# Optimization experiments

Hardware: AMD Instinct MI355X
Metric: run time of the kernel (lower is better)

The kernel has to match this reference:

```python
import jax, jax.numpy as jnp
import numpy as np

LAMDA = 0.05
BETA = 1.0
FULL = 256          # full image / k-space size
SAMP = 128          # sampled k-space size
OFF_R, OFF_C = 3, 3 # sampling offsets from cop.Sample(3, 3, ...)
IR = (OFF_R + 2 * jnp.arange(SAMP)) % FULL  # row sample indices (stride 2)
IC = (OFF_C + 2 * jnp.arange(SAMP)) % FULL  # col sample indices


def dwt2(x):
    # single-level orthonormal 2D Haar DWT, quadrant layout [LL LH; HL HH]
    a = x[..., ::2, ::2]; b = x[..., ::2, 1::2]
    c = x[..., 1::2, ::2]; d = x[..., 1::2, 1::2]
    ll = (a + b + c + d) * 0.5
    lh = (a - b + c - d) * 0.5
    hl = (a + b - c - d) * 0.5
    hh = (a - b - c + d) * 0.5
    top = jnp.concatenate([ll, lh], axis=-1)
    bot = jnp.concatenate([hl, hh], axis=-1)
    return jnp.concatenate([top, bot], axis=-2)


def idwt2(w):
    H = w.shape[-2] // 2; W = w.shape[-1] // 2
    ll = w[..., :H, :W]; lh = w[..., :H, W:]
    hl = w[..., H:, :W]; hh = w[..., H:, W:]
    a = (ll + lh + hl + hh) * 0.5
    b = (ll - lh + hl - hh) * 0.5
    c = (ll + lh - hl - hh) * 0.5
    d = (ll - lh - hl + hh) * 0.5
    x = jnp.zeros(w.shape, w.dtype)
    x = x.at[..., ::2, ::2].set(a)
    x = x.at[..., ::2, 1::2].set(b)
    x = x.at[..., 1::2, ::2].set(c)
    x = x.at[..., 1::2, 1::2].set(d)
    return x


def shrink(x, t):
    # soft-thresholding (prox of t*|x|_1)
    return jnp.sign(x) * jnp.maximum(jnp.abs(x) - t, 0.0)


def sample(x):
    # gather strided k-space samples: [..., 256, 256] -> [..., 128, 128]
    return x[..., IR[:, None], IC[None, :]]


def sample_t(v):
    # adjoint: scatter samples back into zero-filled full grid
    full = jnp.zeros(v.shape[:-2] + (FULL, FULL), v.dtype)
    return full.at[..., IR[:, None], IC[None, :]].set(v)


def setup_inputs() -> dict:
    key = jax.random.key(0)
    k1, k2 = jax.random.split(key)
    s = jax.random.normal(k1, (256, SAMP, SAMP), dtype=jnp.float32)
    image = jax.random.normal(k2, (256, FULL, FULL), dtype=jnp.float32)
    return {"s": s, "image": image}


def reference(s, image):
    thresh = 1.0 / BETA
    coeff = LAMDA / BETA
    dwt_x = dwt2(image)
    new_alpha = shrink(dwt_x, thresh)
    # new_v = dwt_x - new_alpha; idwt(new_alpha - new_v) = idwt(2*alpha - dwt_x)
    idwtx = idwt2(2.0 * new_alpha - dwt_x)
    y = jnp.fft.fft2(idwtx) + coeff * sample_t(s)
    y = y + coeff * sample_t(sample(y))
    return jnp.fft.ifft2(y)
```

## Files before the change

kernel.cpp:

```cpp
#include <hip/hip_runtime.h>


__device__ __forceinline__ float fwv(float w) {
    float sh = fmaxf(fabsf(w) - 1.0f, 0.0f);
    return 2.0f * copysignf(sh, w) - w;
}

__device__ __forceinline__ int bitrev7(int x) {
    return (int)(__builtin_bitreverse32((unsigned)x) >> 25);
}

__global__ __launch_bounds__(1024, 4) void fused_kernel(const float* __restrict__ s,
                                                        const float* __restrict__ image,
                                                        float* __restrict__ outf)
{
    __shared__ float2 A[128 * 128];
    __shared__ float2 ph_tab[256];

    const int tid  = threadIdx.x;
    const int lane = tid & 63;
    const int wave = tid >> 6;
    const int b    = blockIdx.x;
    const float PI_F   = 3.14159265358979323846f;
    const float TWO_PI = 6.2831853071795864769f;

    const float2* ib2 = (const float2*)(image + (size_t)b * 65536);
    const int q  = tid & 63;
    const int pw = tid >> 6;
    float2 img[4][8];
    #pragma unroll
    for (int it = 0; it < 4; ++it) {
        int p = (it << 4) | pw;
        #pragma unroll
        for (int Aq = 0; Aq < 2; ++Aq)
            #pragma unroll
            for (int Bq = 0; Bq < 2; ++Bq)
                #pragma unroll
                for (int r = 0; r < 2; ++r)
                    img[it][(Aq << 2) | (Bq << 1) | r] =
                        ib2[(2 * (p + 64 * Aq) + r) * 128 + (q + 64 * Bq)];
    }

    if (tid < 256) {
        float ps, pc;
        __sincosf((TWO_PI * 3.0f / 256.0f) * (float)tid, &ps, &pc);
        ph_tab[tid] = make_float2(pc, ps);
    }

    float twc[7], tws[7];
    #pragma unroll
    for (int k = 0; k < 7; ++k) {
        int h = 64 >> k;
        float th = PI_F * (float)(lane & (h - 1)) / (float)h;
        __sincosf(th, &tws[k], &twc[k]);
    }

#define FFT128()                                                                     \
    do {                                                                             \
        { float ar = x0r, ai = x0i, br = x1r, bi = x1i;                              \
          x0r = ar + br; x0i = ai + bi;                                              \
          float dr = ar - br, di = ai - bi;                                          \
          x1r = dr * twc[0] - di * tws[0];                                           \
          x1i = dr * tws[0] + di * twc[0]; }                                         \
        _Pragma("unroll")                                                            \
        for (int k = 1; k < 7; ++k) {                                                \
            int h = 64 >> k;                                                         \
            bool hi = (lane & h) != 0;                                               \
            float wc = twc[k], ws = tws[k];                                          \
            { float rr = __shfl_xor(x0r, h), ri = __shfl_xor(x0i, h);                \
              float sr = hi ? (rr - x0r) : (x0r + rr);                               \
              float si = hi ? (ri - x0i) : (x0i + ri);                               \
              float tr = sr * wc - si * ws, ti = sr * ws + si * wc;                  \
              x0r = hi ? tr : sr; x0i = hi ? ti : si; }                              \
            { float rr = __shfl_xor(x1r, h), ri = __shfl_xor(x1i, h);                \
              float sr = hi ? (rr - x1r) : (x1r + rr);                               \
              float si = hi ? (ri - x1i) : (x1i + ri);                               \
              float tr = sr * wc - si * ws, ti = sr * ws + si * wc;                  \
              x1r = hi ? tr : sr; x1i = hi ? ti : si; }                              \
        }                                                                            \
    } while (0)

    const float* sb = s + (size_t)b * (128 * 128);
    const int p0 = lane, p1 = 64 | lane;

    const int m6   = (int)(__builtin_bitreverse32((unsigned)lane) >> 26);
    const int prt0 = (int)(__builtin_bitreverse32((unsigned)((64 - m6) & 63)) >> 26);

    #pragma unroll 2
    for (int t = 0; t < 4; ++t) {
        int ia = (wave << 3) | (t << 1);
        int ic = ia | 1;
        float x0r = sb[ia * 128 + lane];
        float x0i = sb[ic * 128 + lane];
        float x1r = sb[ia * 128 + 64 + lane];
        float x1i = sb[ic * 128 + 64 + lane];
        FFT128();
        float c0r = __shfl(x0r, prt0), c0i = __shfl(x0i, prt0);
        float a0r = 0.5f * (x0r + c0r), a0i = 0.5f * (x0i - c0i);
        float b0r = 0.5f * (x0i + c0i), b0i = 0.5f * (c0r - x0r);
        float c1r = __shfl_xor(x1r, 63), c1i = __shfl_xor(x1i, 63);
        float a1r = 0.5f * (x1r + c1r), a1i = 0.5f * (x1i - c1i);
        float b1r = 0.5f * (x1i + c1i), b1i = 0.5f * (c1r - x1r);
        A[p0 * 128 + ((ia ^ p0) & 127)] = make_float2(a0r, a0i);
        A[p0 * 128 + ((ic ^ p0) & 127)] = make_float2(b0r, b0i);
        A[p1 * 128 + ((ia ^ p1) & 127)] = make_float2(a1r, a1i);
        A[p1 * 128 + ((ic ^ p1) & 127)] = make_float2(b1r, b1i);
    }
    __syncthreads();

    #pragma unroll 2
    for (int t = 0; t < 8; ++t) {
        int vp = (wave << 3) | t;
        float2 a0 = A[vp * 128 + ((p0 ^ vp) & 127)];
        float2 a1 = A[vp * 128 + ((p1 ^ vp) & 127)];
        float x0r = a0.x, x0i = a0.y, x1r = a1.x, x1i = a1.y;
        FFT128();
        A[vp * 128 + ((p0 ^ vp) & 127)] = make_float2(x0r, x0i);
        A[vp * 128 + ((p1 ^ vp) & 127)] = make_float2(x1r, x1i);
    }
    __syncthreads();

    const float  c0    = 0.0125f;
    const float  kappa = 0.0525f / 65536.0f;
    const size_t obase = (size_t)b * 65536;
    const int rv0 = bitrev7(2 * q), rv1 = bitrev7(2 * q + 1);

    #pragma unroll
    for (int it = 0; it < 4; ++it) {
        int p = (it << 4) | pw;

        float D[2][2][2][2];
        #pragma unroll
        for (int Aq = 0; Aq < 2; ++Aq) {
            #pragma unroll
            for (int Bq = 0; Bq < 2; ++Bq) {
                float2 t0 = img[it][(Aq << 2) | (Bq << 1)];
                float2 t1 = img[it][(Aq << 2) | (Bq << 1) | 1];
                float a = t0.x, bb = t0.y, cc = t1.x, dd = t1.y;
                float wll = (a + bb + cc + dd) * 0.5f;
                float wlh = (a - bb + cc - dd) * 0.5f;
                float whl = (a + bb - cc - dd) * 0.5f;
                float whh = (a - bb - cc + dd) * 0.5f;
                float vll = fwv(wll), vlh = fwv(wlh), vhl = fwv(whl), vhh = fwv(whh);
                D[Aq][Bq][0][0] = (vll + vlh + vhl + vhh) * 0.5f;
                D[Aq][Bq][0][1] = (vll - vlh + vhl - vhh) * 0.5f;
                D[Aq][Bq][1][0] = (vll + vlh - vhl - vhh) * 0.5f;
                D[Aq][Bq][1][1] = (vll - vlh - vhl + vhh) * 0.5f;
            }
        }
        float S[2][2];
        #pragma unroll
        for (int r = 0; r < 2; ++r)
            #pragma unroll
            for (int c = 0; c < 2; ++c)
                S[r][c] = D[0][0][r][c] - D[1][0][r][c] - D[0][1][r][c] + D[1][1][r][c];

        int ru0 = bitrev7(2 * p), ru1 = bitrev7(2 * p + 1);
        float2 Tv[2][2];
        Tv[0][0] = A[rv0 * 128 + ((ru0 ^ rv0) & 127)];
        Tv[0][1] = A[rv1 * 128 + ((ru0 ^ rv1) & 127)];
        Tv[1][0] = A[rv0 * 128 + ((ru1 ^ rv0) & 127)];
        Tv[1][1] = A[rv1 * 128 + ((ru1 ^ rv1) & 127)];

        int tbase = 2 * p + 2 * q;
        float2 phv[3] = { ph_tab[tbase], ph_tab[tbase + 1], ph_tab[tbase + 2] };

        #pragma unroll
        for (int Aq = 0; Aq < 2; ++Aq) {
            #pragma unroll
            for (int Bq = 0; Bq < 2; ++Bq) {
                float kq = ((Aq + Bq) & 1) ? -kappa : kappa;
                float sS = ((Aq ^ Bq) & 1) ? -c0 : c0;
                int nrow = 2 * p + 128 * Aq;
                int mcol = 2 * q + 128 * Bq;
                #pragma unroll
                for (int r = 0; r < 2; ++r) {
                    float2 ph0 = phv[r];
                    float2 ph1 = phv[r + 1];
                    float2 wv;
                    wv.x = D[Aq][Bq][r][0] + sS * S[r][0]
                         + kq * (ph0.x * Tv[r][0].x - ph0.y * Tv[r][0].y);
                    wv.y = D[Aq][Bq][r][1] + sS * S[r][1]
                         + kq * (ph1.x * Tv[r][1].x - ph1.y * Tv[r][1].y);
                    *(float2*)&outf[obase + (size_t)((nrow + r) * 256 + mcol)] = wv;
                }
            }
        }
    }
#undef FFT128
}

extern "C" void kernel_launch(void* const* d_in, const int* in_sizes, int n_in,
                              void* d_out, int out_size, void* d_ws, size_t ws_size,
                              hipStream_t stream)
{
    const float* s     = (const float*)d_in[0];
    const float* image = (const float*)d_in[1];
    float*       outf  = (float*)d_out;
    hipLaunchKernelGGL(fused_kernel, dim3(256), dim3(1024), 0, stream,
                       s, image, outf);
}
```

Baseline: 138.8 us.

## Exploit Hermitian symmetry to halve second-pass FFTs and split image loads

The row FFT pass stores only the non-redundant half of each row's spectrum, the column FFT pass runs on only half the rows (paired real columns packed into a complex FFT), and the output stage reads mirrored entries with conjugate sign flips. The image load is split in two: half is loaded up front and the other half after the FFT stage, and the wavelet/shrink work for the first half is computed before the column FFTs. The aim is to halve column-FFT work and reduce register pressure, at the cost of more complex indexing and a special-case branch for the DC/Nyquist pair.

Result: faster. 133.9 us (-3.5%).

```diff
diff --git a/kernel.cpp b/kernel.cpp
--- a/kernel.cpp
+++ b/kernel.cpp
@@ -5,7 +5,6 @@
     float sh = fmaxf(fabsf(w) - 1.0f, 0.0f);
     return 2.0f * copysignf(sh, w) - w;
 }
-
 __device__ __forceinline__ int bitrev7(int x) {
     return (int)(__builtin_bitreverse32((unsigned)x) >> 25);
 }
@@ -25,11 +24,11 @@
     const float TWO_PI = 6.2831853071795864769f;
 
     const float2* ib2 = (const float2*)(image + (size_t)b * 65536);
-    const int q  = tid & 63;
-    const int pw = tid >> 6;
-    float2 img[4][8];
-    #pragma unroll
-    for (int it = 0; it < 4; ++it) {
+    const int q  = lane;
+    const int pw = wave;
+    float2 img01[2][8];
+    #pragma unroll
+    for (int it = 0; it < 2; ++it) {
         int p = (it << 4) | pw;
         #pragma unroll
         for (int Aq = 0; Aq < 2; ++Aq)
@@ -37,7 +36,7 @@
             for (int Bq = 0; Bq < 2; ++Bq)
                 #pragma unroll
                 for (int r = 0; r < 2; ++r)
-                    img[it][(Aq << 2) | (Bq << 1) | r] =
+                    img01[it][(Aq << 2) | (Bq << 1) | r] =
                         ib2[(2 * (p + 64 * Aq) + r) * 128 + (q + 64 * Bq)];
     }
 
@@ -86,6 +85,9 @@
     const int m6   = (int)(__builtin_bitreverse32((unsigned)lane) >> 26);
     const int prt0 = (int)(__builtin_bitreverse32((unsigned)((64 - m6) & 63)) >> 26);
 
+    const bool st0 = ((lane & 1) == 0) || (lane == 1);
+    const bool st1 = ((lane & 1) == 0);
+
     #pragma unroll 2
     for (int t = 0; t < 4; ++t) {
         int ia = (wave << 3) | (t << 1);
@@ -101,41 +103,28 @@
         float c1r = __shfl_xor(x1r, 63), c1i = __shfl_xor(x1i, 63);
         float a1r = 0.5f * (x1r + c1r), a1i = 0.5f * (x1i - c1i);
         float b1r = 0.5f * (x1i + c1i), b1i = 0.5f * (c1r - x1r);
-        A[p0 * 128 + ((ia ^ p0) & 127)] = make_float2(a0r, a0i);
-        A[p0 * 128 + ((ic ^ p0) & 127)] = make_float2(b0r, b0i);
-        A[p1 * 128 + ((ia ^ p1) & 127)] = make_float2(a1r, a1i);
-        A[p1 * 128 + ((ic ^ p1) & 127)] = make_float2(b1r, b1i);
+        if (st0) {
+            A[p0 * 128 + ((ia ^ p0) & 127)] = make_float2(a0r, a0i);
+            A[p0 * 128 + ((ic ^ p0) & 127)] = make_float2(b0r, b0i);
+        }
+        if (st1) {
+            A[p1 * 128 + ((ia ^ p1) & 127)] = make_float2(a1r, a1i);
+            A[p1 * 128 + ((ic ^ p1) & 127)] = make_float2(b1r, b1i);
+        }
     }
     __syncthreads();
 
-    #pragma unroll 2
-    for (int t = 0; t < 8; ++t) {
-        int vp = (wave << 3) | t;
-        float2 a0 = A[vp * 128 + ((p0 ^ vp) & 127)];
-        float2 a1 = A[vp * 128 + ((p1 ^ vp) & 127)];
-        float x0r = a0.x, x0i = a0.y, x1r = a1.x, x1i = a1.y;
-        FFT128();
-        A[vp * 128 + ((p0 ^ vp) & 127)] = make_float2(x0r, x0i);
-        A[vp * 128 + ((p1 ^ vp) & 127)] = make_float2(x1r, x1i);
-    }
-    __syncthreads();
-
-    const float  c0    = 0.0125f;
-    const float  kappa = 0.0525f / 65536.0f;
-    const size_t obase = (size_t)b * 65536;
-    const int rv0 = bitrev7(2 * q), rv1 = bitrev7(2 * q + 1);
-
-    #pragma unroll
-    for (int it = 0; it < 4; ++it) {
-        int p = (it << 4) | pw;
-
+    const float c0c = 0.0125f;
+    float2 base01[2][2][2][2];
+    #pragma unroll
+    for (int it = 0; it < 2; ++it) {
         float D[2][2][2][2];
         #pragma unroll
-        for (int Aq = 0; Aq < 2; ++Aq) {
+        for (int Aq = 0; Aq < 2; ++Aq)
             #pragma unroll
             for (int Bq = 0; Bq < 2; ++Bq) {
-                float2 t0 = img[it][(Aq << 2) | (Bq << 1)];
-                float2 t1 = img[it][(Aq << 2) | (Bq << 1) | 1];
+                float2 t0 = img01[it][(Aq << 2) | (Bq << 1)];
+                float2 t1 = img01[it][(Aq << 2) | (Bq << 1) | 1];
                 float a = t0.x, bb = t0.y, cc = t1.x, dd = t1.y;
                 float wll = (a + bb + cc + dd) * 0.5f;
                 float wlh = (a - bb + cc - dd) * 0.5f;
@@ -147,45 +136,143 @@
                 D[Aq][Bq][1][0] = (vll + vlh - vhl - vhh) * 0.5f;
                 D[Aq][Bq][1][1] = (vll - vlh - vhl + vhh) * 0.5f;
             }
-        }
-        float S[2][2];
-        #pragma unroll
-        for (int r = 0; r < 2; ++r)
-            #pragma unroll
-            for (int c = 0; c < 2; ++c)
-                S[r][c] = D[0][0][r][c] - D[1][0][r][c] - D[0][1][r][c] + D[1][1][r][c];
-
-        int ru0 = bitrev7(2 * p), ru1 = bitrev7(2 * p + 1);
+        #pragma unroll
+        for (int r = 0; r < 2; ++r) {
+            float S0 = D[0][0][r][0] - D[1][0][r][0] - D[0][1][r][0] + D[1][1][r][0];
+            float S1 = D[0][0][r][1] - D[1][0][r][1] - D[0][1][r][1] + D[1][1][r][1];
+            #pragma unroll
+            for (int Aq = 0; Aq < 2; ++Aq)
+                #pragma unroll
+                for (int Bq = 0; Bq < 2; ++Bq) {
+                    float sS = ((Aq ^ Bq) & 1) ? -c0c : c0c;
+                    base01[it][Aq][Bq][r] =
+                        make_float2(D[Aq][Bq][r][0] + sS * S0, D[Aq][Bq][r][1] + sS * S1);
+                }
+        }
+    }
+
+    #pragma unroll 2
+    for (int t = 0; t < 4; ++t) {
+        int vp = (wave << 3) | (t << 1);
+        if (vp == 0) {
+            float x0r = A[p0].x, x0i = A[128 + (p0 ^ 1)].x;
+            float x1r = A[p1].x, x1i = A[128 + (p1 ^ 1)].x;
+            FFT128();
+            float c0r = __shfl(x0r, prt0), c0i = __shfl(x0i, prt0);
+            float T0r = 0.5f * (x0r + c0r), T0i = 0.5f * (x0i - c0i);
+            float S0r = 0.5f * (x0i + c0i), S0i = 0.5f * (c0r - x0r);
+            float c1r = __shfl_xor(x1r, 63), c1i = __shfl_xor(x1i, 63);
+            float T1r = 0.5f * (x1r + c1r), T1i = 0.5f * (x1i - c1i);
+            float S1r = 0.5f * (x1i + c1i), S1i = 0.5f * (c1r - x1r);
+            A[p0] = make_float2(T0r, T0i);
+            A[p1] = make_float2(T1r, T1i);
+            A[128 + (p0 ^ 1)] = make_float2(S0r, S0i);
+            A[128 + (p1 ^ 1)] = make_float2(S1r, S1i);
+        } else {
+            float2 a0 = A[vp * 128 + ((p0 ^ vp) & 127)];
+            float2 a1 = A[vp * 128 + ((p1 ^ vp) & 127)];
+            float x0r = a0.x, x0i = a0.y, x1r = a1.x, x1i = a1.y;
+            FFT128();
+            A[vp * 128 + ((p0 ^ vp) & 127)] = make_float2(x0r, x0i);
+            A[vp * 128 + ((p1 ^ vp) & 127)] = make_float2(x1r, x1i);
+        }
+    }
+    __syncthreads();
+
+    float2 img23[2][8];
+    #pragma unroll
+    for (int it = 0; it < 2; ++it) {
+        int p = ((it + 2) << 4) | pw;
+        #pragma unroll
+        for (int Aq = 0; Aq < 2; ++Aq)
+            #pragma unroll
+            for (int Bq = 0; Bq < 2; ++Bq)
+                #pragma unroll
+                for (int r = 0; r < 2; ++r)
+                    img23[it][(Aq << 2) | (Bq << 1) | r] =
+                        ib2[(2 * (p + 64 * Aq) + r) * 128 + (q + 64 * Bq)];
+    }
+
+    const float  kappa = 0.0525f / 65536.0f;
+    const size_t obase = (size_t)b * 65536;
+
+    const int  v0c = 2 * q, v1c = 2 * q + 1;
+    const bool f0 = v0c > 64, f1 = v1c > 64;
+    const int  rv0 = bitrev7(f0 ? 128 - v0c : v0c);
+    const int  rv1 = bitrev7(f1 ? 128 - v1c : v1c);
+    const float sg0 = f0 ? -1.0f : 1.0f;
+    const float sg1 = f1 ? -1.0f : 1.0f;
+
+    auto emit = [&](int p, const float2 (&bse)[2][2][2]) {
         float2 Tv[2][2];
-        Tv[0][0] = A[rv0 * 128 + ((ru0 ^ rv0) & 127)];
-        Tv[0][1] = A[rv1 * 128 + ((ru0 ^ rv1) & 127)];
-        Tv[1][0] = A[rv0 * 128 + ((ru1 ^ rv0) & 127)];
-        Tv[1][1] = A[rv1 * 128 + ((ru1 ^ rv1) & 127)];
-
-        int tbase = 2 * p + 2 * q;
-        float2 phv[3] = { ph_tab[tbase], ph_tab[tbase + 1], ph_tab[tbase + 2] };
-
-        #pragma unroll
-        for (int Aq = 0; Aq < 2; ++Aq) {
+        #pragma unroll
+        for (int r = 0; r < 2; ++r) {
+            int u   = 2 * p + r;
+            int ruD = bitrev7(u);
+            int ruC = bitrev7((128 - u) & 127);
+            float2 t0 = A[rv0 * 128 + (((f0 ? ruC : ruD) ^ rv0) & 127)];
+            float2 t1 = A[rv1 * 128 + (((f1 ? ruC : ruD) ^ rv1) & 127)];
+            Tv[r][0] = make_float2(t0.x, sg0 * t0.y);
+            Tv[r][1] = make_float2(t1.x, sg1 * t1.y);
+        }
+        int tb = 2 * p + 2 * q;
+        float2 phv[3] = { ph_tab[tb], ph_tab[tb + 1], ph_tab[tb + 2] };
+        #pragma unroll
+        for (int Aq = 0; Aq < 2; ++Aq)
             #pragma unroll
             for (int Bq = 0; Bq < 2; ++Bq) {
                 float kq = ((Aq + Bq) & 1) ? -kappa : kappa;
-                float sS = ((Aq ^ Bq) & 1) ? -c0 : c0;
                 int nrow = 2 * p + 128 * Aq;
                 int mcol = 2 * q + 128 * Bq;
                 #pragma unroll
                 for (int r = 0; r < 2; ++r) {
-                    float2 ph0 = phv[r];
-                    float2 ph1 = phv[r + 1];
+                    float2 ph0 = phv[r], ph1 = phv[r + 1];
                     float2 wv;
-                    wv.x = D[Aq][Bq][r][0] + sS * S[r][0]
-                         + kq * (ph0.x * Tv[r][0].x - ph0.y * Tv[r][0].y);
-                    wv.y = D[Aq][Bq][r][1] + sS * S[r][1]
-                         + kq * (ph1.x * Tv[r][1].x - ph1.y * Tv[r][1].y);
+                    wv.x = bse[Aq][Bq][r].x + kq * (ph0.x * Tv[r][0].x - ph0.y * Tv[r][0].y);
+                    wv.y = bse[Aq][Bq][r].y + kq * (ph1.x * Tv[r][1].x - ph1.y * Tv[r][1].y);
                     *(float2*)&outf[obase + (size_t)((nrow + r) * 256 + mcol)] = wv;
                 }
             }
-        }
+    };
+
+    emit((0 << 4) | pw, base01[0]);
+    emit((1 << 4) | pw, base01[1]);
+
+    #pragma unroll
+    for (int it = 0; it < 2; ++it) {
+        float D[2][2][2][2];
+        #pragma unroll
+        for (int Aq = 0; Aq < 2; ++Aq)
+            #pragma unroll
+            for (int Bq = 0; Bq < 2; ++Bq) {
+                float2 t0 = img23[it][(Aq << 2) | (Bq << 1)];
+                float2 t1 = img23[it][(Aq << 2) | (Bq << 1) | 1];
+                float a = t0.x, bb = t0.y, cc = t1.x, dd = t1.y;
+                float wll = (a + bb + cc + dd) * 0.5f;
+                float wlh = (a - bb + cc - dd) * 0.5f;
+                float whl = (a + bb - cc - dd) * 0.5f;
+                float whh = (a - bb - cc + dd) * 0.5f;
+                float vll = fwv(wll), vlh = fwv(wlh), vhl = fwv(whl), vhh = fwv(whh);
+                D[Aq][Bq][0][0] = (vll + vlh + vhl + vhh) * 0.5f;
+                D[Aq][Bq][0][1] = (vll - vlh + vhl - vhh) * 0.5f;
+                D[Aq][Bq][1][0] = (vll + vlh - vhl - vhh) * 0.5f;
+                D[Aq][Bq][1][1] = (vll - vlh - vhl + vhh) * 0.5f;
+            }
+        float2 bse[2][2][2];
+        #pragma unroll
+        for (int r = 0; r < 2; ++r) {
+            float S0 = D[0][0][r][0] - D[1][0][r][0] - D[0][1][r][0] + D[1][1][r][0];
+            float S1 = D[0][0][r][1] - D[1][0][r][1] - D[0][1][r][1] + D[1][1][r][1];
+            #pragma unroll
+            for (int Aq = 0; Aq < 2; ++Aq)
+                #pragma unroll
+                for (int Bq = 0; Bq < 2; ++Bq) {
+                    float sS = ((Aq ^ Bq) & 1) ? -c0c : c0c;
+                    bse[Aq][Bq][r] =
+                        make_float2(D[Aq][Bq][r][0] + sS * S0, D[Aq][Bq][r][1] + sS * S1);
+                }
+        }
+        emit(((it + 2) << 4) | pw, bse);
     }
 #undef FFT128
 }
```
